# Performance work log

Measured on AMD Instinct MI355X. Metric: run time of the kernel, lower is better.

Reference implementation:

```python
import jax, jax.numpy as jnp
import numpy as np

B, S, D = 8, 2048, 1024

def setup_inputs() -> dict:
    key = jax.random.key(0)
    ks = jax.random.split(key, 9)
    s = 1.0 / np.sqrt(D)
    return {
        "x": jax.random.normal(ks[0], (B, S, D), dtype=jnp.float32),
        "Wq": jax.random.uniform(ks[1], (D, D), jnp.float32, -s, s),
        "bq": jax.random.uniform(ks[2], (D,), jnp.float32, -s, s),
        "Wk": jax.random.uniform(ks[3], (D, D), jnp.float32, -s, s),
        "bk": jax.random.uniform(ks[4], (D,), jnp.float32, -s, s),
        "Wv": jax.random.uniform(ks[5], (D, D), jnp.float32, -s, s),
        "bv": jax.random.uniform(ks[6], (D,), jnp.float32, -s, s),
        "Wo": jax.random.uniform(ks[7], (D, 1), jnp.float32, -s, s),
        "bo": jax.random.uniform(ks[8], (1,), jnp.float32, -s, s),
    }

def reference(x, Wq, bq, Wk, bk, Wv, bv, Wo, bo):
    q = x @ Wq + bq                      # [B,S,D]
    k = x @ Wk + bk                      # [B,S,D]
    v = x @ Wv + bv                      # [B,S,D]
    scores = jnp.einsum('bsd,btd->bst', q, k)   # [B,S,S], NOTE: no 1/sqrt(D) scaling in source
    attn = jax.nn.softmax(scores, axis=-1)
    out = jnp.einsum('bst,btd->bsd', attn, v)   # [B,S,D]
    return out @ Wo + bo                 # [B,S,1]
```

## Files before the change

### kernel.cpp

```cpp
#include <hip/hip_runtime.h>
#include <stdint.h>

#define D_ 1024
#define S_ 2048
#define B_ 8

typedef _Float16 h16;
typedef _Float16 f16x8 __attribute__((ext_vector_type(8)));
typedef _Float16 f16x4 __attribute__((ext_vector_type(4)));
typedef float    f32x4 __attribute__((ext_vector_type(4)));

typedef __attribute__((address_space(3))) void lds_void;
typedef const __attribute__((address_space(1))) void g_void;

#define MFMA16(a, b, c) __builtin_amdgcn_mfma_f32_16x16x32_f16(a, b, c, 0, 0, 0)
#define VMCNT(n) asm volatile("s_waitcnt vmcnt(" #n ")" ::: "memory")
#define SFENCE() __builtin_amdgcn_sched_barrier(0)
#define SBAR() __builtin_amdgcn_s_barrier()

__device__ __forceinline__ void stage16(const h16* g0, int ld, h16* lchunk) {
  int lane = threadIdx.x & 63;
  int c = (lane & 3) ^ ((lane >> 3) & 3);
  const h16* ga = g0 + (size_t)(lane >> 2) * ld + c * 8;
  __builtin_amdgcn_global_load_lds((g_void*)ga, (lds_void*)lchunk, 16, 0, 0);
}

__global__ void k_u(const float* __restrict__ Wv, const float* __restrict__ Wo,
                    const float* __restrict__ bv, float* __restrict__ u) {
  int lane = threadIdx.x & 63;
  if (blockIdx.x == 256) {
    if (threadIdx.x < 64) {
      float s = 0.f;
      #pragma unroll
      for (int j = 0; j < 4; ++j) {
        float4 a = ((const float4*)bv)[j * 64 + lane];
        float4 b = ((const float4*)Wo)[j * 64 + lane];
        s += a.x * b.x + a.y * b.y + a.z * b.z + a.w * b.w;
      }
      #pragma unroll
      for (int off = 32; off; off >>= 1) s += __shfl_xor(s, off, 64);
      if (lane == 0) u[D_] = s;
    }
    return;
  }
  int row = blockIdx.x * 4 + (threadIdx.x >> 6);
  const float4* r4 = (const float4*)(Wv + (size_t)row * D_);
  const float4* w4 = (const float4*)Wo;
  float s = 0.f;
  #pragma unroll
  for (int j = 0; j < 4; ++j) {
    int c = j * 64 + lane;
    float4 a = r4[c], b = w4[c];
    s += a.x * b.x + a.y * b.y + a.z * b.z + a.w * b.w;
  }
  #pragma unroll
  for (int off = 32; off; off >>= 1) s += __shfl_xor(s, off, 64);
  if (lane == 0) u[row] = s;
}

__global__ void k_wt(const float* __restrict__ Wq, const float* __restrict__ Wk,
                     h16* __restrict__ Wt) {
  __shared__ float t[32][33];
  int n0 = blockIdx.x * 32;
  int k0 = blockIdx.y * 32;
  const float* src = (n0 < D_) ? Wq : Wk;
  int nn = n0 & (D_ - 1);
  int tx = threadIdx.x, ty = threadIdx.y;
  for (int i = ty; i < 32; i += 8)
    t[i][tx] = src[(size_t)(k0 + i) * D_ + nn + tx];
  __syncthreads();
  for (int i = ty; i < 32; i += 8)
    Wt[(size_t)(n0 + i) * D_ + k0 + tx] = (h16)t[tx][i];
}

__global__ void k_xw(const float* __restrict__ x, const float* __restrict__ u,
                     h16* __restrict__ xh, float* __restrict__ w) {
  int row = blockIdx.x * 4 + (threadIdx.x >> 6);
  int lane = threadIdx.x & 63;
  const float4* xr = (const float4*)(x + (size_t)row * D_);
  const float4* u4 = (const float4*)u;
  h16* xo = xh + (size_t)row * D_;
  float s = 0.f;
  #pragma unroll
  for (int j = 0; j < 4; ++j) {
    int c = j * 64 + lane;
    float4 a = xr[c];
    float4 b = u4[c];
    s += a.x * b.x + a.y * b.y + a.z * b.z + a.w * b.w;
    f16x4 o;
    o[0] = (h16)a.x; o[1] = (h16)a.y; o[2] = (h16)a.z; o[3] = (h16)a.w;
    *(f16x4*)(xo + c * 4) = o;
  }
  #pragma unroll
  for (int off = 32; off; off >>= 1) s += __shfl_xor(s, off, 64);
  if (lane == 0) w[row] = s + u[D_];
}

__global__ __launch_bounds__(256, 4) void k_proj(
    const h16* __restrict__ xh, const h16* __restrict__ Wt,
    const float* __restrict__ bq_, const float* __restrict__ bk_,
    h16* __restrict__ qkh) {
  __shared__ alignas(16) h16 As[2][128 * 32];
  __shared__ alignas(16) h16 Bs[2][128 * 32];
  int tid = threadIdx.x;
  int w = tid >> 6;
  int lane = tid & 63;
  int wr = w >> 1, wc = w & 1;
  int g = lane >> 4, l15 = lane & 15;
  int swz = (l15 >> 1) & 3;

  int idx = (blockIdx.x & 7) * 256 + (blockIdx.x >> 3);
  int m0 = (idx >> 4) * 128, n0 = (idx & 15) * 128;

  f32x4 acc[4][4] = {};

  #define STAGE_PROJ(buf, k)                                                    \
    {                                                                           \
      int k0_ = (k) * 32;                                                       \
      _Pragma("unroll")                                                         \
      for (int j = 0; j < 2; ++j) {                                             \
        int ch = w * 2 + j;                                                     \
        stage16(xh + (size_t)(m0 + ch * 16) * D_ + k0_, D_, &As[buf][ch * 512]);\
        stage16(Wt + (size_t)(n0 + ch * 16) * D_ + k0_, D_, &Bs[buf][ch * 512]);\
      }                                                                         \
    }

  STAGE_PROJ(0, 0);
  for (int k = 0; k < 32; ++k) {
    int buf = k & 1;
    if (k + 1 < 32) {
      STAGE_PROJ(buf ^ 1, k + 1);
      VMCNT(4);
    } else {
      VMCNT(0);
    }
    SFENCE();
    SBAR();
    SFENCE();
    f16x8 af[4], bf[4];
    #pragma unroll
    for (int i = 0; i < 4; ++i) {
      af[i] = *(const f16x8*)(&As[buf][(wr * 64 + i * 16 + l15) * 32 + (g ^ swz) * 8]);
      bf[i] = *(const f16x8*)(&Bs[buf][(wc * 64 + i * 16 + l15) * 32 + (g ^ swz) * 8]);
    }
    __builtin_amdgcn_s_setprio(1);
    #pragma unroll
    for (int mi = 0; mi < 4; ++mi)
      #pragma unroll
      for (int ni = 0; ni < 4; ++ni)
        acc[mi][ni] = MFMA16(af[mi], bf[ni], acc[mi][ni]);
    __builtin_amdgcn_s_setprio(0);
    SBAR();
  }

  #pragma unroll
  for (int ni = 0; ni < 4; ++ni) {
    int n = n0 + wc * 64 + ni * 16 + l15;
    float bias = (n < D_) ? bq_[n] : bk_[n - D_];
    #pragma unroll
    for (int mi = 0; mi < 4; ++mi) {
      #pragma unroll
      for (int r = 0; r < 4; ++r) {
        int m = m0 + wr * 64 + mi * 16 + g * 4 + r;
        qkh[(size_t)m * (2 * D_) + n] = (h16)(acc[mi][ni][r] + bias);
      }
    }
  }
}

__global__ __launch_bounds__(512, 4) void k_attn(
    const h16* __restrict__ qkh, const float* __restrict__ wv,
    float* __restrict__ part) {
  __shared__ alignas(16) h16 Qs[2][64 * 32];
  __shared__ alignas(16) h16 Ks[2][512 * 32];
  __shared__ float sm[3][8][64];
  int tid = threadIdx.x;
  int w = tid >> 6;
  int lane = tid & 63;
  int g = lane >> 4, l15 = lane & 15;
  int swz = (l15 >> 1) & 3;
  int b = blockIdx.x & 7;
  int h = (blockIdx.x >> 3) & 1;
  int q0 = (blockIdx.x >> 4) * 64;
  int t0 = h * 1024;
  size_t rbase = (size_t)b * S_;

  #define STAGE_ATTN(buf, st)                                                   \
    {                                                                           \
      int tt_ = (st) >> 5, k0_ = ((st) & 31) * 32;                              \
      _Pragma("unroll")                                                         \
      for (int j = 0; j < 4; ++j) {                                             \
        int ck = w * 4 + j;                                                     \
        stage16(qkh + (rbase + t0 + tt_ * 512 + ck * 16) * (2 * D_) + D_ + k0_, \
                2 * D_, &Ks[buf][ck * 512]);                                    \
      }                                                                         \
      if (w < 4)                                                                \
        stage16(qkh + (rbase + q0 + w * 16) * (2 * D_) + k0_,                   \
                2 * D_, &Qs[buf][w * 512]);                                     \
    }

  float mrun[4][4], num[4][4], den[4][4];
  #pragma unroll
  for (int mi = 0; mi < 4; ++mi)
    #pragma unroll
    for (int r = 0; r < 4; ++r) { mrun[mi][r] = -1e30f; num[mi][r] = 0.f; den[mi][r] = 0.f; }

  STAGE_ATTN(0, 0);

  for (int tt = 0; tt < 2; ++tt) {
    f32x4 acc[4][4] = {};
    for (int kc = 0; kc < 32; ++kc) {
      int st = tt * 32 + kc, buf = st & 1;
      if (st + 1 < 64) {
        STAGE_ATTN(buf ^ 1, st + 1);
        if (w < 4) { VMCNT(5); } else { VMCNT(4); }
      } else {
        VMCNT(0);
      }
      SFENCE();
      SBAR();
      SFENCE();
      f16x8 qf[4], kf[4];
      #pragma unroll
      for (int i = 0; i < 4; ++i) {
        qf[i] = *(const f16x8*)(&Qs[buf][(i * 16 + l15) * 32 + (g ^ swz) * 8]);
        kf[i] = *(const f16x8*)(&Ks[buf][(w * 64 + i * 16 + l15) * 32 + (g ^ swz) * 8]);
      }
      __builtin_amdgcn_s_setprio(1);
      #pragma unroll
      for (int mi = 0; mi < 4; ++mi)
        #pragma unroll
        for (int ni = 0; ni < 4; ++ni)
          acc[mi][ni] = MFMA16(qf[mi], kf[ni], acc[mi][ni]);
      __builtin_amdgcn_s_setprio(0);
      SBAR();
    }
    float wvv[4];
    #pragma unroll
    for (int ni = 0; ni < 4; ++ni)
      wvv[ni] = wv[rbase + t0 + tt * 512 + w * 64 + ni * 16 + l15];
    #pragma unroll
    for (int mi = 0; mi < 4; ++mi) {
      #pragma unroll
      for (int r = 0; r < 4; ++r) {
        float v = fmaxf(fmaxf(acc[mi][0][r], acc[mi][1][r]),
                        fmaxf(acc[mi][2][r], acc[mi][3][r]));
        #pragma unroll
        for (int off = 1; off < 16; off <<= 1) v = fmaxf(v, __shfl_xor(v, off, 64));
        float mn = fmaxf(mrun[mi][r], v);
        float scl = __expf(mrun[mi][r] - mn);
        float pn = 0.f, pd = 0.f;
        #pragma unroll
        for (int ni = 0; ni < 4; ++ni) {
          float p = __expf(acc[mi][ni][r] - mn);
          pn += p * wvv[ni];
          pd += p;
        }
        num[mi][r] = num[mi][r] * scl + pn;
        den[mi][r] = den[mi][r] * scl + pd;
        mrun[mi][r] = mn;
      }
    }
  }
  #pragma unroll
  for (int mi = 0; mi < 4; ++mi)
    #pragma unroll
    for (int r = 0; r < 4; ++r) {
      #pragma unroll
      for (int off = 1; off < 16; off <<= 1) {
        num[mi][r] += __shfl_xor(num[mi][r], off, 64);
        den[mi][r] += __shfl_xor(den[mi][r], off, 64);
      }
    }
  if (l15 == 0) {
    #pragma unroll
    for (int mi = 0; mi < 4; ++mi)
      #pragma unroll
      for (int r = 0; r < 4; ++r) {
        int row = mi * 16 + g * 4 + r;
        sm[0][w][row] = mrun[mi][r];
        sm[1][w][row] = num[mi][r];
        sm[2][w][row] = den[mi][r];
      }
  }
  __syncthreads();
  if (tid < 64) {
    float M = sm[0][0][tid];
    #pragma unroll
    for (int j = 1; j < 8; ++j) M = fmaxf(M, sm[0][j][tid]);
    float N = 0.f, Dn = 0.f;
    #pragma unroll
    for (int j = 0; j < 8; ++j) {
      float e = __expf(sm[0][j][tid] - M);
      N += sm[1][j][tid] * e;
      Dn += sm[2][j][tid] * e;
    }
    size_t row = rbase + q0 + tid;
    part[row * 6 + h * 3 + 0] = M;
    part[row * 6 + h * 3 + 1] = N;
    part[row * 6 + h * 3 + 2] = Dn;
  }
}

__global__ void k_fin(const float* __restrict__ part, const float* __restrict__ bo,
                      float* __restrict__ out) {
  int idx = blockIdx.x * 256 + threadIdx.x;
  if (idx >= B_ * S_) return;
  float m1 = part[idx * 6 + 0], n1 = part[idx * 6 + 1], d1 = part[idx * 6 + 2];
  float m2 = part[idx * 6 + 3], n2 = part[idx * 6 + 4], d2 = part[idx * 6 + 5];
  float M = fmaxf(m1, m2);
  float e1 = __expf(m1 - M), e2 = __expf(m2 - M);
  out[idx] = (n1 * e1 + n2 * e2) / (d1 * e1 + d2 * e2) + bo[0];
}

extern "C" void kernel_launch(void* const* d_in, const int* in_sizes, int n_in,
                              void* d_out, int out_size, void* d_ws, size_t ws_size,
                              hipStream_t stream) {
  const float* x  = (const float*)d_in[0];
  const float* Wq = (const float*)d_in[1];
  const float* bq = (const float*)d_in[2];
  const float* Wk = (const float*)d_in[3];
  const float* bk = (const float*)d_in[4];
  const float* Wv = (const float*)d_in[5];
  const float* bv = (const float*)d_in[6];
  const float* Wo = (const float*)d_in[7];
  const float* bo = (const float*)d_in[8];
  float* out = (float*)d_out;

  char* ws = (char*)d_ws;
  h16*   xh   = (h16*)ws;
  h16*   Wt   = (h16*)(ws + (size_t)32 * 1024 * 1024);
  h16*   qkh  = (h16*)(ws + (size_t)36 * 1024 * 1024);
  float* wv   = (float*)(ws + (size_t)100 * 1024 * 1024);
  float* u    = (float*)(ws + (size_t)100 * 1024 * 1024 + 65536);
  float* part = (float*)(ws + (size_t)101 * 1024 * 1024);

  hipLaunchKernelGGL(k_u,    dim3(257),    dim3(256),   0, stream, Wv, Wo, bv, u);
  hipLaunchKernelGGL(k_wt,   dim3(64, 32), dim3(32, 8), 0, stream, Wq, Wk, Wt);
  hipLaunchKernelGGL(k_xw,   dim3(4096),   dim3(256),   0, stream, x, u, xh, wv);
  hipLaunchKernelGGL(k_proj, dim3(2048),   dim3(256),   0, stream, xh, Wt, bq, bk, qkh);
  hipLaunchKernelGGL(k_attn, dim3(512),    dim3(512),   0, stream, qkh, wv, part);
  hipLaunchKernelGGL(k_fin,  dim3(64),     dim3(256),   0, stream, part, bo, out);
}
```

Measured before the change: 329.0 us.

## Retile projection and attention kernels into 2D warp grids with 8-way key split

The projection GEMM now uses 512-thread blocks covering 256x128 output tiles, with warps arranged 4x2. This halves the number of blocks and increases reuse of the staged B tile. The attention kernel is restructured from 64 queries against 1024 keys per block into 128 queries against 256 keys, using a 2x4 warp grid. Key chunks are split 8 ways, so each block does one single-pass softmax partial and drops the running max rescaling. The finalize kernel merges 8 partials instead of 2. The grid doubles and the partial buffer grows, trading more combine work for better Q/K reuse and more parallelism.

```diff
diff --git a/kernel.cpp b/kernel.cpp
--- a/kernel.cpp
+++ b/kernel.cpp
@@ -96,41 +96,43 @@
   if (lane == 0) w[row] = s + u[D_];
 }
 
-__global__ __launch_bounds__(256, 4) void k_proj(
+__global__ __launch_bounds__(512, 4) void k_proj(
     const h16* __restrict__ xh, const h16* __restrict__ Wt,
     const float* __restrict__ bq_, const float* __restrict__ bk_,
     h16* __restrict__ qkh) {
-  __shared__ alignas(16) h16 As[2][128 * 32];
+  __shared__ alignas(16) h16 As[2][256 * 32];
   __shared__ alignas(16) h16 Bs[2][128 * 32];
   int tid = threadIdx.x;
   int w = tid >> 6;
   int lane = tid & 63;
-  int wr = w >> 1, wc = w & 1;
+  int wrow = w >> 1, wcol = w & 1;
   int g = lane >> 4, l15 = lane & 15;
   int swz = (l15 >> 1) & 3;
 
-  int idx = (blockIdx.x & 7) * 256 + (blockIdx.x >> 3);
-  int m0 = (idx >> 4) * 128, n0 = (idx & 15) * 128;
+  int idx = (blockIdx.x & 7) * 128 + (blockIdx.x >> 3);
+  int m0 = (idx >> 4) * 256, n0 = (idx & 15) * 128;
+
+  const h16* abase0 = xh + (size_t)(m0 + (2 * w) * 16) * D_;
+  const h16* abase1 = abase0 + (size_t)16 * D_;
+  const h16* bbase  = Wt + (size_t)(n0 + w * 16) * D_;
 
   f32x4 acc[4][4] = {};
 
-  #define STAGE_PROJ(buf, k)                                                    \
-    {                                                                           \
-      int k0_ = (k) * 32;                                                       \
-      _Pragma("unroll")                                                         \
-      for (int j = 0; j < 2; ++j) {                                             \
-        int ch = w * 2 + j;                                                     \
-        stage16(xh + (size_t)(m0 + ch * 16) * D_ + k0_, D_, &As[buf][ch * 512]);\
-        stage16(Wt + (size_t)(n0 + ch * 16) * D_ + k0_, D_, &Bs[buf][ch * 512]);\
-      }                                                                         \
+  #define STAGE_PROJ(buf, k)                                          \
+    {                                                                 \
+      int k0_ = (k) * 32;                                             \
+      stage16(abase0 + k0_, D_, &As[buf][(2 * w) * 512]);             \
+      stage16(abase1 + k0_, D_, &As[buf][(2 * w + 1) * 512]);         \
+      stage16(bbase + k0_, D_, &Bs[buf][w * 512]);                    \
     }
 
   STAGE_PROJ(0, 0);
+  #pragma unroll 2
   for (int k = 0; k < 32; ++k) {
     int buf = k & 1;
     if (k + 1 < 32) {
       STAGE_PROJ(buf ^ 1, k + 1);
-      VMCNT(4);
+      VMCNT(3);
     } else {
       VMCNT(0);
     }
@@ -140,8 +142,8 @@
     f16x8 af[4], bf[4];
     #pragma unroll
     for (int i = 0; i < 4; ++i) {
-      af[i] = *(const f16x8*)(&As[buf][(wr * 64 + i * 16 + l15) * 32 + (g ^ swz) * 8]);
-      bf[i] = *(const f16x8*)(&Bs[buf][(wc * 64 + i * 16 + l15) * 32 + (g ^ swz) * 8]);
+      af[i] = *(const f16x8*)(&As[buf][(wrow * 64 + i * 16 + l15) * 32 + (g ^ swz) * 8]);
+      bf[i] = *(const f16x8*)(&Bs[buf][(wcol * 64 + i * 16 + l15) * 32 + (g ^ swz) * 8]);
     }
     __builtin_amdgcn_s_setprio(1);
     #pragma unroll
@@ -155,13 +157,13 @@
 
   #pragma unroll
   for (int ni = 0; ni < 4; ++ni) {
-    int n = n0 + wc * 64 + ni * 16 + l15;
+    int n = n0 + wcol * 64 + ni * 16 + l15;
     float bias = (n < D_) ? bq_[n] : bk_[n - D_];
     #pragma unroll
     for (int mi = 0; mi < 4; ++mi) {
       #pragma unroll
       for (int r = 0; r < 4; ++r) {
-        int m = m0 + wr * 64 + mi * 16 + g * 4 + r;
+        int m = m0 + wrow * 64 + mi * 16 + g * 4 + r;
         qkh[(size_t)m * (2 * D_) + n] = (h16)(acc[mi][ni][r] + bias);
       }
     }
@@ -171,134 +173,112 @@
 __global__ __launch_bounds__(512, 4) void k_attn(
     const h16* __restrict__ qkh, const float* __restrict__ wv,
     float* __restrict__ part) {
-  __shared__ alignas(16) h16 Qs[2][64 * 32];
-  __shared__ alignas(16) h16 Ks[2][512 * 32];
-  __shared__ float sm[3][8][64];
+  __shared__ alignas(16) h16 Qs[2][128 * 32];
+  __shared__ alignas(16) h16 Ks[2][256 * 32];
+  __shared__ float sm[3][4][128];
   int tid = threadIdx.x;
   int w = tid >> 6;
   int lane = tid & 63;
   int g = lane >> 4, l15 = lane & 15;
   int swz = (l15 >> 1) & 3;
+  int wq = w >> 2, wkc = w & 3;
   int b = blockIdx.x & 7;
-  int h = (blockIdx.x >> 3) & 1;
-  int q0 = (blockIdx.x >> 4) * 64;
-  int t0 = h * 1024;
+  int r = blockIdx.x >> 3;
+  int kc = r >> 4;
+  int q0 = (r & 15) * 128;
   size_t rbase = (size_t)b * S_;
 
-  #define STAGE_ATTN(buf, st)                                                   \
-    {                                                                           \
-      int tt_ = (st) >> 5, k0_ = ((st) & 31) * 32;                              \
-      _Pragma("unroll")                                                         \
-      for (int j = 0; j < 4; ++j) {                                             \
-        int ck = w * 4 + j;                                                     \
-        stage16(qkh + (rbase + t0 + tt_ * 512 + ck * 16) * (2 * D_) + D_ + k0_, \
-                2 * D_, &Ks[buf][ck * 512]);                                    \
-      }                                                                         \
-      if (w < 4)                                                                \
-        stage16(qkh + (rbase + q0 + w * 16) * (2 * D_) + k0_,                   \
-                2 * D_, &Qs[buf][w * 512]);                                     \
-    }
-
-  float mrun[4][4], num[4][4], den[4][4];
-  #pragma unroll
-  for (int mi = 0; mi < 4; ++mi)
-    #pragma unroll
-    for (int r = 0; r < 4; ++r) { mrun[mi][r] = -1e30f; num[mi][r] = 0.f; den[mi][r] = 0.f; }
+  const h16* qbase  = qkh + (rbase + q0 + w * 16) * (2 * D_);
+  const h16* kbase0 = qkh + (rbase + kc * 256 + (2 * w) * 16) * (2 * D_) + D_;
+  const h16* kbase1 = kbase0 + (size_t)16 * (2 * D_);
+
+  #define STAGE_ATTN(buf, st)                                         \
+    {                                                                 \
+      int k0_ = (st) * 32;                                            \
+      stage16(qbase + k0_, 2 * D_, &Qs[buf][w * 512]);                \
+      stage16(kbase0 + k0_, 2 * D_, &Ks[buf][(2 * w) * 512]);         \
+      stage16(kbase1 + k0_, 2 * D_, &Ks[buf][(2 * w + 1) * 512]);     \
+    }
+
+  f32x4 acc[4][4] = {};
 
   STAGE_ATTN(0, 0);
-
-  for (int tt = 0; tt < 2; ++tt) {
-    f32x4 acc[4][4] = {};
-    for (int kc = 0; kc < 32; ++kc) {
-      int st = tt * 32 + kc, buf = st & 1;
-      if (st + 1 < 64) {
-        STAGE_ATTN(buf ^ 1, st + 1);
-        if (w < 4) { VMCNT(5); } else { VMCNT(4); }
-      } else {
-        VMCNT(0);
-      }
-      SFENCE();
-      SBAR();
-      SFENCE();
-      f16x8 qf[4], kf[4];
-      #pragma unroll
-      for (int i = 0; i < 4; ++i) {
-        qf[i] = *(const f16x8*)(&Qs[buf][(i * 16 + l15) * 32 + (g ^ swz) * 8]);
-        kf[i] = *(const f16x8*)(&Ks[buf][(w * 64 + i * 16 + l15) * 32 + (g ^ swz) * 8]);
-      }
-      __builtin_amdgcn_s_setprio(1);
-      #pragma unroll
-      for (int mi = 0; mi < 4; ++mi)
-        #pragma unroll
-        for (int ni = 0; ni < 4; ++ni)
-          acc[mi][ni] = MFMA16(qf[mi], kf[ni], acc[mi][ni]);
-      __builtin_amdgcn_s_setprio(0);
-      SBAR();
-    }
-    float wvv[4];
-    #pragma unroll
-    for (int ni = 0; ni < 4; ++ni)
-      wvv[ni] = wv[rbase + t0 + tt * 512 + w * 64 + ni * 16 + l15];
-    #pragma unroll
-    for (int mi = 0; mi < 4; ++mi) {
-      #pragma unroll
-      for (int r = 0; r < 4; ++r) {
-        float v = fmaxf(fmaxf(acc[mi][0][r], acc[mi][1][r]),
-                        fmaxf(acc[mi][2][r], acc[mi][3][r]));
-        #pragma unroll
-        for (int off = 1; off < 16; off <<= 1) v = fmaxf(v, __shfl_xor(v, off, 64));
-        float mn = fmaxf(mrun[mi][r], v);
-        float scl = __expf(mrun[mi][r] - mn);
-        float pn = 0.f, pd = 0.f;
-        #pragma unroll
-        for (int ni = 0; ni < 4; ++ni) {
-          float p = __expf(acc[mi][ni][r] - mn);
-          pn += p * wvv[ni];
-          pd += p;
-        }
-        num[mi][r] = num[mi][r] * scl + pn;
-        den[mi][r] = den[mi][r] * scl + pd;
-        mrun[mi][r] = mn;
-      }
-    }
-  }
-  #pragma unroll
-  for (int mi = 0; mi < 4; ++mi)
-    #pragma unroll
-    for (int r = 0; r < 4; ++r) {
+  #pragma unroll 2
+  for (int st = 0; st < 32; ++st) {
+    int buf = st & 1;
+    if (st + 1 < 32) {
+      STAGE_ATTN(buf ^ 1, st + 1);
+      VMCNT(3);
+    } else {
+      VMCNT(0);
+    }
+    SFENCE();
+    SBAR();
+    SFENCE();
+    f16x8 qf[4], kf[4];
+    #pragma unroll
+    for (int i = 0; i < 4; ++i) {
+      qf[i] = *(const f16x8*)(&Qs[buf][(wq * 64 + i * 16 + l15) * 32 + (g ^ swz) * 8]);
+      kf[i] = *(const f16x8*)(&Ks[buf][(wkc * 64 + i * 16 + l15) * 32 + (g ^ swz) * 8]);
+    }
+    __builtin_amdgcn_s_setprio(1);
+    #pragma unroll
+    for (int mi = 0; mi < 4; ++mi)
+      #pragma unroll
+      for (int ni = 0; ni < 4; ++ni)
+        acc[mi][ni] = MFMA16(qf[mi], kf[ni], acc[mi][ni]);
+    __builtin_amdgcn_s_setprio(0);
+    SBAR();
+  }
+
+  float wvv[4];
+  #pragma unroll
+  for (int ni = 0; ni < 4; ++ni)
+    wvv[ni] = wv[rbase + kc * 256 + wkc * 64 + ni * 16 + l15];
+  #pragma unroll
+  for (int mi = 0; mi < 4; ++mi) {
+    #pragma unroll
+    for (int rr = 0; rr < 4; ++rr) {
+      float v = fmaxf(fmaxf(acc[mi][0][rr], acc[mi][1][rr]),
+                      fmaxf(acc[mi][2][rr], acc[mi][3][rr]));
+      #pragma unroll
+      for (int off = 1; off < 16; off <<= 1) v = fmaxf(v, __shfl_xor(v, off, 64));
+      float pn = 0.f, pd = 0.f;
+      #pragma unroll
+      for (int ni = 0; ni < 4; ++ni) {
+        float p = __expf(acc[mi][ni][rr] - v);
+        pn += p * wvv[ni];
+        pd += p;
+      }
       #pragma unroll
       for (int off = 1; off < 16; off <<= 1) {
-        num[mi][r] += __shfl_xor(num[mi][r], off, 64);
-        den[mi][r] += __shfl_xor(den[mi][r], off, 64);
-      }
-    }
-  if (l15 == 0) {
-    #pragma unroll
-    for (int mi = 0; mi < 4; ++mi)
-      #pragma unroll
-      for (int r = 0; r < 4; ++r) {
-        int row = mi * 16 + g * 4 + r;
-        sm[0][w][row] = mrun[mi][r];
-        sm[1][w][row] = num[mi][r];
-        sm[2][w][row] = den[mi][r];
-      }
+        pn += __shfl_xor(pn, off, 64);
+        pd += __shfl_xor(pd, off, 64);
+      }
+      if (l15 == 0) {
+        int row = wq * 64 + mi * 16 + g * 4 + rr;
+        sm[0][wkc][row] = v;
+        sm[1][wkc][row] = pn;
+        sm[2][wkc][row] = pd;
+      }
+    }
   }
   __syncthreads();
-  if (tid < 64) {
+  if (tid < 128) {
     float M = sm[0][0][tid];
     #pragma unroll
-    for (int j = 1; j < 8; ++j) M = fmaxf(M, sm[0][j][tid]);
+    for (int j = 1; j < 4; ++j) M = fmaxf(M, sm[0][j][tid]);
     float N = 0.f, Dn = 0.f;
     #pragma unroll
-    for (int j = 0; j < 8; ++j) {
+    for (int j = 0; j < 4; ++j) {
       float e = __expf(sm[0][j][tid] - M);
       N += sm[1][j][tid] * e;
       Dn += sm[2][j][tid] * e;
     }
     size_t row = rbase + q0 + tid;
-    part[row * 6 + h * 3 + 0] = M;
-    part[row * 6 + h * 3 + 1] = N;
-    part[row * 6 + h * 3 + 2] = Dn;
+    part[row * 24 + kc * 3 + 0] = M;
+    part[row * 24 + kc * 3 + 1] = N;
+    part[row * 24 + kc * 3 + 2] = Dn;
   }
 }
 
@@ -306,11 +286,18 @@
                       float* __restrict__ out) {
   int idx = blockIdx.x * 256 + threadIdx.x;
   if (idx >= B_ * S_) return;
-  float m1 = part[idx * 6 + 0], n1 = part[idx * 6 + 1], d1 = part[idx * 6 + 2];
-  float m2 = part[idx * 6 + 3], n2 = part[idx * 6 + 4], d2 = part[idx * 6 + 5];
-  float M = fmaxf(m1, m2);
-  float e1 = __expf(m1 - M), e2 = __expf(m2 - M);
-  out[idx] = (n1 * e1 + n2 * e2) / (d1 * e1 + d2 * e2) + bo[0];
+  const float* p = part + (size_t)idx * 24;
+  float M = p[0];
+  #pragma unroll
+  for (int j = 1; j < 8; ++j) M = fmaxf(M, p[j * 3]);
+  float N = 0.f, Dn = 0.f;
+  #pragma unroll
+  for (int j = 0; j < 8; ++j) {
+    float e = __expf(p[j * 3] - M);
+    N += p[j * 3 + 1] * e;
+    Dn += p[j * 3 + 2] * e;
+  }
+  out[idx] = N / Dn + bo[0];
 }
 
 extern "C" void kernel_launch(void* const* d_in, const int* in_sizes, int n_in,
@@ -338,7 +325,7 @@
   hipLaunchKernelGGL(k_u,    dim3(257),    dim3(256),   0, stream, Wv, Wo, bv, u);
   hipLaunchKernelGGL(k_wt,   dim3(64, 32), dim3(32, 8), 0, stream, Wq, Wk, Wt);
   hipLaunchKernelGGL(k_xw,   dim3(4096),   dim3(256),   0, stream, x, u, xh, wv);
-  hipLaunchKernelGGL(k_proj, dim3(2048),   dim3(256),   0, stream, xh, Wt, bq, bk, qkh);
-  hipLaunchKernelGGL(k_attn, dim3(512),    dim3(512),   0, stream, qkh, wv, part);
+  hipLaunchKernelGGL(k_proj, dim3(1024),   dim3(512),   0, stream, xh, Wt, bq, bk, qkh);
+  hipLaunchKernelGGL(k_attn, dim3(1024),   dim3(512),   0, stream, qkh, wv, part);
   hipLaunchKernelGGL(k_fin,  dim3(64),     dim3(256),   0, stream, part, bo, out);
 }
```

New measurement: 282.4 us. -14.1%, faster.
